# Kernel optimization log

Measured on AMD Instinct MI355X. Metric: run time of the kernel, lower is better.

Reference implementation:

```python
import jax, jax.numpy as jnp
import numpy as np

N_ATOMS = 100_000
N_EDGES = 200_000
N_LG = 400_000
N_GRAPHS = 1024
ATOM_FDIM = 39
BOND_FDIM = 11
HIDDEN = 300
DEPTH = 6


def setup_inputs() -> dict:
    key = jax.random.key(0)
    ks = jax.random.split(key, 10)
    atom_features = jax.random.normal(ks[0], (N_ATOMS, ATOM_FDIM), jnp.float32)
    bond_features = jax.random.normal(ks[1], (N_EDGES, BOND_FDIM), jnp.float32)
    edge_src = jax.random.randint(ks[2], (N_EDGES,), 0, N_ATOMS)
    edge_dst = jax.random.randint(ks[3], (N_EDGES,), 0, N_ATOMS)
    lg_src = jax.random.randint(ks[4], (N_LG,), 0, N_EDGES)
    lg_dst = jax.random.randint(ks[5], (N_LG,), 0, N_EDGES)
    # deterministic balanced assignment of atoms to graphs (every graph non-empty)
    graph_ids = (jnp.arange(N_ATOMS) * N_GRAPHS) // N_ATOMS
    fan_in = ATOM_FDIM + BOND_FDIM
    W_i = jax.random.normal(ks[6], (fan_in, HIDDEN), jnp.float32) * (1.0 / np.sqrt(fan_in))
    W_h = jax.random.normal(ks[7], (HIDDEN, HIDDEN), jnp.float32) * (1.0 / np.sqrt(HIDDEN))
    W_o = jax.random.normal(ks[8], (ATOM_FDIM + HIDDEN, HIDDEN), jnp.float32) * (1.0 / np.sqrt(ATOM_FDIM + HIDDEN))
    b_o = jax.random.normal(ks[9], (HIDDEN,), jnp.float32) * 0.01
    return {
        'atom_features': atom_features, 'bond_features': bond_features,
        'W_i': W_i, 'W_h': W_h, 'W_o': W_o, 'b_o': b_o,
        'edge_src': edge_src, 'edge_dst': edge_dst,
        'lg_src': lg_src, 'lg_dst': lg_dst, 'graph_ids': graph_ids,
    }


def reference(atom_features, bond_features, W_i, W_h, W_o, b_o,
              edge_src, edge_dst, lg_src, lg_dst, graph_ids):
    # line-graph node features: [source atom feats | bond feats] -> W_i
    feats = jnp.concatenate([atom_features[edge_src], bond_features], axis=1)  # [E, 50]
    msg_input = feats @ W_i                                                    # [E, H]
    msg = jax.nn.relu(msg_input)

    # loopy BP: depth-1 iterations of gather-sum over line-graph edges + linear + relu
    def step(msg, _):
        accum = jax.ops.segment_sum(msg[lg_src], lg_dst, num_segments=N_EDGES)  # [E, H]
        return jax.nn.relu(msg_input + accum @ W_h), None
    msg, _ = jax.lax.scan(step, msg, None, length=DEPTH - 1)

    # gather edge messages into destination atoms, then GatherUpdate
    m = jax.ops.segment_sum(msg, edge_dst, num_segments=N_ATOMS)               # [N, H]
    h = jax.nn.relu(jnp.concatenate([atom_features, m], axis=1) @ W_o + b_o)   # [N, H]

    # per-graph mean pooling
    sums = jax.ops.segment_sum(h, graph_ids, num_segments=N_GRAPHS)            # [G, H]
    counts = jax.ops.segment_sum(jnp.ones((N_ATOMS, 1), h.dtype), graph_ids, num_segments=N_GRAPHS)
    return sums / jnp.maximum(counts, 1.0)
```

## Files before the change

### kernel.cpp

```cpp
#include <hip/hip_runtime.h>
#include <stdint.h>

#define NA 100000
#define NE 200000
#define NLG 400000
#define NG 1024
#define AF 39
#define BFD 11
#define HID 300
#define DEPTH 6

#define E_PAD 200064
#define A_PAD 100096
#define EG 12504
#define AGR 6250
#define AG2 6256
#define MS 304
#define NT 20

typedef unsigned short u16;
typedef __attribute__((ext_vector_type(8))) short s8v;
typedef __attribute__((ext_vector_type(8))) unsigned short u16x8;
typedef __attribute__((ext_vector_type(4))) float f4v;

__device__ inline u16 f2bf(float x){
  unsigned u = __float_as_uint(x);
  u += 0x7FFFu + ((u>>16)&1u);
  return (u16)(u>>16);
}
__device__ inline float bf2f(u16 b){ return __uint_as_float(((unsigned)b)<<16); }

#define GLOAD_LDS16(gp, lp) __builtin_amdgcn_global_load_lds( \
    (const __attribute__((address_space(1))) void*)(gp), \
    (__attribute__((address_space(3))) void*)(lp), 16, 0, 0)

__global__ void prep_whi(const float* __restrict__ Wi, const float* __restrict__ Wh,
                         u16* __restrict__ Wf){
  int idx = blockIdx.x*256 + threadIdx.x;
  const int total = 12*NT*512;
  if (idx >= total) return;
  int j    = idx & 7;
  int lane = (idx>>3) & 63;
  int tile = idx >> 9;
  int nt = tile % NT, kt = tile / NT;
  int k = kt*32 + ((lane>>4)<<3) + j;
  int n = nt*16 + (lane&15);
  float v = 0.f;
  if (n < HID){
    if (k < AF+BFD) v = Wi[(size_t)k*HID + n];
    else if (k >= 64 && k < 64+HID) v = Wh[(size_t)(k-64)*HID + n];
  }
  Wf[idx] = f2bf(v);
}

__global__ void prep_wo(const float* __restrict__ W, u16* __restrict__ Wf){
  int idx = blockIdx.x*256 + threadIdx.x;
  const int total = 11*NT*512;
  if (idx >= total) return;
  int j    = idx & 7;
  int lane = (idx>>3) & 63;
  int tile = idx >> 9;
  int nt = tile % NT, kt = tile / NT;
  int k = kt*32 + ((lane>>4)<<3) + j;
  int n = nt*16 + (lane&15);
  int ks = (k < AF) ? k : ((k >= 48 && k < 348) ? (k-9) : -1);
  float v = 0.f;
  if (ks >= 0 && n < HID) v = W[(size_t)ks*HID + n];
  Wf[idx] = f2bf(v);
}

__global__ void hist_k(const int* __restrict__ dst, int* __restrict__ cnt, int n){
  int i = blockIdx.x*256 + threadIdx.x;
  if (i < n) atomicAdd(&cnt[dst[i]], 1);
}
__global__ void scan1(const int* __restrict__ cnt, int* __restrict__ off,
                      int* __restrict__ part, int n){
  __shared__ int s[256];
  const int t = threadIdx.x, b = blockIdx.x;
  const int i0 = b*1024 + t*4;
  int v0 = (i0+0<n)?cnt[i0+0]:0, v1=(i0+1<n)?cnt[i0+1]:0, v2=(i0+2<n)?cnt[i0+2]:0, v3=(i0+3<n)?cnt[i0+3]:0;
  int sum = v0+v1+v2+v3;
  s[t]=sum; __syncthreads();
  for (int o=1;o<256;o<<=1){ int x=(t>=o)?s[t-o]:0; __syncthreads(); s[t]+=x; __syncthreads(); }
  int excl = s[t]-sum;
  if (i0+0<n) off[i0+0]=excl;
  if (i0+1<n) off[i0+1]=excl+v0;
  if (i0+2<n) off[i0+2]=excl+v0+v1;
  if (i0+3<n) off[i0+3]=excl+v0+v1+v2;
  if (t==255) part[b]=s[255];
}
__global__ void scan2(const int* __restrict__ part, int* __restrict__ pref, int nblk){
  __shared__ int s[256];
  const int t = threadIdx.x;
  int v = (t<nblk)?part[t]:0;
  s[t]=v; __syncthreads();
  for (int o=1;o<256;o<<=1){ int x=(t>=o)?s[t-o]:0; __syncthreads(); s[t]+=x; __syncthreads(); }
  pref[t] = s[t]-v;
}
__global__ void scan3(int* __restrict__ off, const int* __restrict__ pref,
                      const int* __restrict__ part, int n, int nblk){
  const int t = threadIdx.x, b = blockIdx.x;
  const int i0 = b*1024 + t*4;
  const int p = pref[b];
  #pragma unroll
  for (int k=0;k<4;++k) if (i0+k<n) off[i0+k]+=p;
  if (b==0 && t==0) off[n] = pref[nblk-1] + part[nblk-1];
}
__global__ void scatter_val(const int* __restrict__ dst, const int* __restrict__ src,
                            const int* __restrict__ off, int* __restrict__ cur,
                            int* __restrict__ csr, int n){
  int i = blockIdx.x*256 + threadIdx.x; if (i>=n) return;
  int d = dst[i];
  int p = off[d] + atomicAdd(&cur[d],1);
  csr[p] = src[i];
}
__global__ void scatter_idx(const int* __restrict__ dst, const int* __restrict__ off,
                            int* __restrict__ cur, int* __restrict__ csr, int n){
  int i = blockIdx.x*256 + threadIdx.x; if (i>=n) return;
  int d = dst[i];
  int p = off[d] + atomicAdd(&cur[d],1);
  csr[p] = i;
}

__launch_bounds__(256,3)
__global__ void gather_lg_k(const u16* __restrict__ msg, u16* __restrict__ accf,
                            const int* __restrict__ off, const int* __restrict__ csr){
  const int w = threadIdx.x>>6, lane = threadIdx.x&63;
  const int g16 = blockIdx.x*4 + w;
  if (g16 >= EG) return;
  const int e = g16*16 + (lane&15);
  const int gc = lane>>4;
  int s=0, epos=0;
  if (e < NE){ s = off[e]; epos = off[e+1]; }
  float acc[10][8];
  #pragma unroll
  for (int c=0;c<10;++c)
    #pragma unroll
    for (int j=0;j<8;++j) acc[c][j] = 0.f;
  const bool c9live = (gc < 2);
  for (int it=s; it<epos; ++it){
    const int src = csr[it];
    const u16* base = msg + (size_t)src*MS + gc*8;
    u16x8 v[10];
    #pragma unroll
    for (int c=0;c<9;++c) v[c] = *(const u16x8*)(base + c*32);
    if (c9live) v[9] = *(const u16x8*)(base + 288);
    else { u16x8 z = {0,0,0,0,0,0,0,0}; v[9] = z; }
    #pragma unroll
    for (int c=0;c<10;++c)
      #pragma unroll
      for (int j=0;j<8;++j) acc[c][j] += bf2f(v[c][j]);
  }
  #pragma unroll
  for (int c=0;c<10;++c){
    u16x8 o;
    #pragma unroll
    for (int j=0;j<8;++j) o[j] = f2bf(acc[c][j]);
    *(u16x8*)(accf + ((size_t)g16*10 + c)*512 + lane*8) = o;
  }
}

__launch_bounds__(256,3)
__global__ void gather_at_k(const u16* __restrict__ msg, const float* __restrict__ atomf,
                            u16* __restrict__ atf,
                            const int* __restrict__ off, const int* __restrict__ csr){
  const int w = threadIdx.x>>6, lane = threadIdx.x&63;
  const int g16 = blockIdx.x*4 + w;
  if (g16 >= AGR) return;
  const int a = g16*16 + (lane&15);
  const int gc = lane>>4;
  const int s = off[a], epos = off[a+1];
  float acc[10][8];
  #pragma unroll
  for (int c=0;c<10;++c)
    #pragma unroll
    for (int j=0;j<8;++j) acc[c][j] = 0.f;
  const bool k1live = (gc >= 2);
  for (int it=s; it<epos; ++it){
    const int src = csr[it];
    const u16* base = msg + (size_t)src*MS + gc*8 - 48;
    u16x8 v[10];
    if (k1live) v[0] = *(const u16x8*)(base + 32);
    else { u16x8 z = {0,0,0,0,0,0,0,0}; v[0] = z; }
    #pragma unroll
    for (int kt=2; kt<=10; ++kt) v[kt-1] = *(const u16x8*)(base + kt*32);
    #pragma unroll
    for (int c=0;c<10;++c)
      #pragma unroll
      for (int j=0;j<8;++j) acc[c][j] += bf2f(v[c][j]);
  }
  #pragma unroll
  for (int kt=1; kt<=10; ++kt){
    u16x8 o;
    if (kt==1 && !k1live){
      #pragma unroll
      for (int j=0;j<8;++j){
        const int k = 32 + gc*8 + j;
        o[j] = f2bf((k < AF) ? atomf[(size_t)a*AF + k] : 0.f);
      }
    } else {
      #pragma unroll
      for (int j=0;j<8;++j) o[j] = f2bf(acc[kt-1][j]);
    }
    *(u16x8*)(atf + ((size_t)g16*11 + kt)*512 + lane*8) = o;
  }
}

__global__ void prep_atom(const float* __restrict__ atomf, u16* __restrict__ atf){
  const int w = threadIdx.x>>6, lane = threadIdx.x&63;
  const int g16 = blockIdx.x*4 + w;
  if (g16 >= AGR) return;
  const int a = g16*16 + (lane&15);
  const int gc = lane>>4;
  u16x8 o;
  #pragma unroll
  for (int j=0;j<8;++j) o[j] = f2bf(atomf[(size_t)a*AF + gc*8 + j]);
  *(u16x8*)(atf + ((size_t)g16*11 + 0)*512 + lane*8) = o;
}

template<int MODE>
__launch_bounds__(256,2)
__global__ void gemm_fused(const float* __restrict__ atomf,
                           const float* __restrict__ bondf,
                           const int*   __restrict__ esrc,
                           const u16*   __restrict__ Afrag,
                           const u16*   __restrict__ Bfrag,
                           u16*         __restrict__ msgout,
                           const float* __restrict__ bo,
                           const int*   __restrict__ gids,
                           float*       __restrict__ gout)
{
  constexpr int KT = (MODE==0) ? 2 : (MODE==1 ? 12 : 11);
  __shared__ u16 lds[2][28*512];
  const int t = threadIdx.x, w = t>>6, lane = t&63;
  const int wr = w>>1, wc = w&1;
  const int m0g = blockIdx.x*8;
  const int r16 = lane&15, gc = lane>>4;

  int rowv[2], srcv[2];
  #pragma unroll
  for (int i=0;i<2;++i){
    const int row = (m0g + w*2 + i)*16 + r16;
    rowv[i] = row;
    if constexpr (MODE<=1) srcv[i] = (row < NE) ? esrc[row] : 0;
    else                   srcv[i] = 0;
  }

  f4v acc[4][10];
  const f4v fz = {0.f,0.f,0.f,0.f};
  #pragma unroll
  for (int i=0;i<4;++i)
    #pragma unroll
    for (int n=0;n<10;++n) acc[i][n] = fz;

  auto stageA = [&](int buf, int kt){
    if constexpr (MODE==2){
      #pragma unroll
      for (int i=0;i<2;++i){
        const int rg = m0g + w*2 + i;
        GLOAD_LDS16(Afrag + ((size_t)rg*11 + kt)*512 + lane*8, &lds[buf][(w*2+i)*512]);
      }
    } else {
      if (MODE==1 && kt >= 2){
        #pragma unroll
        for (int i=0;i<2;++i){
          const int rg = m0g + w*2 + i;
          GLOAD_LDS16(Afrag + ((size_t)rg*10 + (kt-2))*512 + lane*8, &lds[buf][(w*2+i)*512]);
        }
      } else {
        #pragma unroll
        for (int i=0;i<2;++i){
          const int row = rowv[i];
          const int src = srcv[i];
          const bool ok = row < NE;
          const int k0  = kt*32 + gc*8;
          u16x8 o;
          #pragma unroll
          for (int j=0;j<8;++j){
            const int k = k0+j;
            float x = 0.f;
            if (ok){
              if (k < AF) x = atomf[(size_t)src*AF + k];
              else if (k < AF+BFD) x = bondf[(size_t)row*BFD + (k-AF)];
            }
            o[j] = f2bf(x);
          }
          *(u16x8*)(&lds[buf][(w*2+i)*512 + lane*8]) = o;
        }
      }
    }
    #pragma unroll
    for (int i=0;i<5;++i){
      const int nt = w*5+i;
      GLOAD_LDS16(Bfrag + ((size_t)kt*NT + nt)*512 + lane*8, &lds[buf][(8+nt)*512]);
    }
  };

  int buf = 0;
  stageA(0, 0);
  __syncthreads();
  for (int kt=0; kt<KT; ++kt){
    if (kt+1 < KT) stageA(buf^1, kt+1);
    s8v a[4];
    #pragma unroll
    for (int i=0;i<4;++i) a[i] = *(const s8v*)&lds[buf][(wr*4+i)*512 + lane*8];
    #pragma unroll
    for (int h2=0; h2<2; ++h2){
      s8v b[5];
      #pragma unroll
      for (int n=0;n<5;++n) b[n] = *(const s8v*)&lds[buf][(8 + wc*10 + h2*5 + n)*512 + lane*8];
      #pragma unroll
      for (int n=0;n<5;++n)
        #pragma unroll
        for (int i=0;i<4;++i)
          acc[i][h2*5+n] = __builtin_amdgcn_mfma_f32_16x16x32_bf16(a[i], b[n], acc[i][h2*5+n], 0,0,0);
    }
    __syncthreads();
    buf ^= 1;
  }

  const int colL = r16;
  const int row0 = m0g*16 + wr*64 + (gc<<2);
  if constexpr (MODE<=1){
    #pragma unroll
    for (int n=0;n<10;++n){
      const int col = wc*160 + n*16 + colL;
      if (col >= MS) continue;
      #pragma unroll
      for (int i=0;i<4;++i)
        #pragma unroll
        for (int r=0;r<4;++r){
          const int row = row0 + i*16 + r;
          const float v = (col < HID) ? fmaxf(acc[i][n][r], 0.f) : 0.f;
          msgout[(size_t)row*MS + col] = f2bf(v);
        }
    }
  } else {
    float* pl = (float*)&lds[0][0];
    for (int idx=t; idx<960; idx+=256) pl[idx] = 0.f;
    __syncthreads();
    const int gb = gids[m0g*16 < NA ? m0g*16 : (NA-1)];
    #pragma unroll
    for (int n=0;n<10;++n){
      const int col = wc*160 + n*16 + colL;
      if (col >= HID) continue;
      const float bv = bo[col];
      #pragma unroll
      for (int i=0;i<4;++i)
        #pragma unroll
        for (int r=0;r<4;++r){
          const int row = row0 + i*16 + r;
          if (row >= NA) continue;
          const float h = fmaxf(acc[i][n][r] + bv, 0.f);
          const int gl = gids[row] - gb;
          atomicAdd(&pl[gl*320 + col], h);
        }
    }
    __syncthreads();
    for (int idx=t; idx<960; idx+=256){
      const int g = idx/320, c = idx - g*320;
      if (c < HID){
        const int gg = gb + g;
        if (gg < NG){
          const float vv = pl[idx];
          if (vv != 0.f) atomicAdd(&gout[(size_t)gg*HID + c], vv);
        }
      }
    }
  }
}

__device__ inline int lbound(const int* a, int n, int v){
  int lo=0, hi=n;
  while (lo<hi){ int m=(lo+hi)>>1; if (a[m]<v) lo=m+1; else hi=m; }
  return lo;
}
__global__ void scale_k(float* __restrict__ out, const int* __restrict__ gids){
  const int g = blockIdx.x, t = threadIdx.x;
  __shared__ int se[2];
  if (t < 2) se[t] = lbound(gids, NA, g+t);
  __syncthreads();
  const float inv = 1.0f / (float)((se[1]-se[0]) > 1 ? (se[1]-se[0]) : 1);
  for (int c=t; c<HID; c+=256)
    out[(size_t)g*HID + c] *= inv;
}

extern "C" void kernel_launch(void* const* d_in, const int* in_sizes, int n_in,
                              void* d_out, int out_size, void* d_ws, size_t ws_size,
                              hipStream_t stream)
{
  const float* atomf = (const float*)d_in[0];
  const float* bondf = (const float*)d_in[1];
  const float* W_i   = (const float*)d_in[2];
  const float* W_h   = (const float*)d_in[3];
  const float* W_o   = (const float*)d_in[4];
  const float* b_o   = (const float*)d_in[5];
  const int*   esrc  = (const int*)d_in[6];
  const int*   edst  = (const int*)d_in[7];
  const int*   lsrc  = (const int*)d_in[8];
  const int*   ldst  = (const int*)d_in[9];
  const int*   gids  = (const int*)d_in[10];

  char* ws = (char*)d_ws;
  size_t wsoff = 0;
  auto walloc = [&](size_t bytes)->void*{
    void* p = ws + wsoff;
    wsoff += (bytes + 1023) & ~(size_t)1023;
    return p;
  };
  u16*  m0    = (u16*) walloc((size_t)E_PAD*MS*2);
  u16*  m1    = (u16*) walloc((size_t)EG*10*1024);
  u16*  atf   = m1;
  u16*  whif  = (u16*) walloc((size_t)12*NT*512*2);
  u16*  wof   = (u16*) walloc((size_t)11*NT*512*2);
  int* off_lg = (int*) walloc((size_t)(NE+1)*4);
  int* csr_lg = (int*) walloc((size_t)NLG*4);
  int* buf_lg = (int*) walloc((size_t)NE*4);
  int* off_at = (int*) walloc((size_t)(NA+1)*4);
  int* csr_at = (int*) walloc((size_t)NE*4);
  int* buf_at = (int*) walloc((size_t)NA*4);
  int* part1  = (int*) walloc(256*4);
  int* pref1  = (int*) walloc(256*4);
  int* part2  = (int*) walloc(256*4);
  int* pref2  = (int*) walloc(256*4);

  if (wsoff > ws_size) return;

  float* gout = (float*)d_out;
  hipMemsetAsync(gout,   0, (size_t)out_size*4, stream);
  hipMemsetAsync(buf_lg, 0, (size_t)NE*4, stream);
  hipMemsetAsync(buf_at, 0, (size_t)NA*4, stream);

  prep_whi<<<480,256,0,stream>>>(W_i, W_h, whif);
  prep_wo <<<440,256,0,stream>>>(W_o, wof);

  hist_k<<<(NLG+255)/256,256,0,stream>>>(ldst, buf_lg, NLG);
  hist_k<<<(NE+255)/256,256,0,stream>>>(edst, buf_at, NE);
  scan1<<<196,256,0,stream>>>(buf_lg, off_lg, part1, NE);
  scan2<<<1,256,0,stream>>>(part1, pref1, 196);
  scan3<<<196,256,0,stream>>>(off_lg, pref1, part1, NE, 196);
  scan1<<<98,256,0,stream>>>(buf_at, off_at, part2, NA);
  scan2<<<1,256,0,stream>>>(part2, pref2, 98);
  scan3<<<98,256,0,stream>>>(off_at, pref2, part2, NA, 98);
  hipMemsetAsync(buf_lg, 0, (size_t)NE*4, stream);
  hipMemsetAsync(buf_at, 0, (size_t)NA*4, stream);
  scatter_val<<<(NLG+255)/256,256,0,stream>>>(ldst, lsrc, off_lg, buf_lg, csr_lg, NLG);
  scatter_idx<<<(NE+255)/256,256,0,stream>>>(edst, off_at, buf_at, csr_at, NE);

  gemm_fused<0><<<E_PAD/128,256,0,stream>>>(atomf, bondf, esrc, nullptr, whif, m0,
                                            nullptr, nullptr, nullptr);

  for (int d=0; d<DEPTH-1; ++d){
    gather_lg_k<<<EG/4,256,0,stream>>>(m0, m1, off_lg, csr_lg);
    gemm_fused<1><<<E_PAD/128,256,0,stream>>>(atomf, bondf, esrc, m1, whif, m0,
                                              nullptr, nullptr, nullptr);
  }

  prep_atom  <<<(AGR+3)/4,256,0,stream>>>(atomf, atf);
  gather_at_k<<<(AGR+3)/4,256,0,stream>>>(m0, atomf, atf, off_at, csr_at);
  gemm_fused<2><<<A_PAD/128,256,0,stream>>>(atomf, bondf, nullptr, atf, wof, nullptr,
                                            b_o, gids, gout);

  scale_k<<<NG,256,0,stream>>>(gout, gids);
}
```

Before: 1.295 ms.

## Load MFMA fragments directly from global into registers and stage output through LDS

Replaces the LDS double-buffered GEMM with one that loads pre-swizzled A and B fragments straight from global memory into registers, fully unrolls the K loop, and prefetches the first two edge-feature K tiles into registers up front. The message-output epilogue now transposes through per-wave LDS so each lane writes contiguous 16-byte row chunks instead of scattered 2-byte stores. Launch bounds drop to one block per SM, allowing more registers. The aim is to remove block-wide barriers and LDS traffic and to coalesce the output writes, at the cost of redundant B-fragment global/L2 reads across waves and possibly lower occupancy.

New measurement: 1.781 ms. +37.6%, slower.

```diff
diff --git a/kernel.cpp b/kernel.cpp
--- a/kernel.cpp
+++ b/kernel.cpp
@@ -14,7 +14,6 @@
 #define A_PAD 100096
 #define EG 12504
 #define AGR 6250
-#define AG2 6256
 #define MS 304
 #define NT 20
 
@@ -29,10 +28,6 @@
   return (u16)(u>>16);
 }
 __device__ inline float bf2f(u16 b){ return __uint_as_float(((unsigned)b)<<16); }
-
-#define GLOAD_LDS16(gp, lp) __builtin_amdgcn_global_load_lds( \
-    (const __attribute__((address_space(1))) void*)(gp), \
-    (__attribute__((address_space(3))) void*)(lp), 16, 0, 0)
 
 __global__ void prep_whi(const float* __restrict__ Wi, const float* __restrict__ Wh,
                          u16* __restrict__ Wf){
@@ -219,33 +214,24 @@
 }
 
 template<int MODE>
-__launch_bounds__(256,2)
-__global__ void gemm_fused(const float* __restrict__ atomf,
-                           const float* __restrict__ bondf,
-                           const int*   __restrict__ esrc,
-                           const u16*   __restrict__ Afrag,
-                           const u16*   __restrict__ Bfrag,
-                           u16*         __restrict__ msgout,
-                           const float* __restrict__ bo,
-                           const int*   __restrict__ gids,
-                           float*       __restrict__ gout)
+__launch_bounds__(256,1)
+__global__ void gemm_reg(const float* __restrict__ atomf,
+                         const float* __restrict__ bondf,
+                         const int*   __restrict__ esrc,
+                         const u16*   __restrict__ Afrag,
+                         const u16*   __restrict__ Bfrag,
+                         u16*         __restrict__ msgout,
+                         const float* __restrict__ bo,
+                         const int*   __restrict__ gids,
+                         float*       __restrict__ gout)
 {
   constexpr int KT = (MODE==0) ? 2 : (MODE==1 ? 12 : 11);
-  __shared__ u16 lds[2][28*512];
+  __shared__ u16 smem[4*64*88];
   const int t = threadIdx.x, w = t>>6, lane = t&63;
   const int wr = w>>1, wc = w&1;
   const int m0g = blockIdx.x*8;
   const int r16 = lane&15, gc = lane>>4;
 
-  int rowv[2], srcv[2];
-  #pragma unroll
-  for (int i=0;i<2;++i){
-    const int row = (m0g + w*2 + i)*16 + r16;
-    rowv[i] = row;
-    if constexpr (MODE<=1) srcv[i] = (row < NE) ? esrc[row] : 0;
-    else                   srcv[i] = 0;
-  }
-
   f4v acc[4][10];
   const f4v fz = {0.f,0.f,0.f,0.f};
   #pragma unroll
@@ -253,93 +239,103 @@
     #pragma unroll
     for (int n=0;n<10;++n) acc[i][n] = fz;
 
-  auto stageA = [&](int buf, int kt){
-    if constexpr (MODE==2){
-      #pragma unroll
-      for (int i=0;i<2;++i){
-        const int rg = m0g + w*2 + i;
-        GLOAD_LDS16(Afrag + ((size_t)rg*11 + kt)*512 + lane*8, &lds[buf][(w*2+i)*512]);
-      }
-    } else {
-      if (MODE==1 && kt >= 2){
+  s8v fa[2][4];
+  if constexpr (MODE<=1){
+    #pragma unroll
+    for (int i=0;i<4;++i){
+      const int rg  = m0g + wr*4 + i;
+      const int row = rg*16 + r16;
+      const bool ok = row < NE;
+      const int src = ok ? esrc[row] : 0;
+      #pragma unroll
+      for (int kt=0; kt<2; ++kt){
+        u16x8 o;
         #pragma unroll
-        for (int i=0;i<2;++i){
-          const int rg = m0g + w*2 + i;
-          GLOAD_LDS16(Afrag + ((size_t)rg*10 + (kt-2))*512 + lane*8, &lds[buf][(w*2+i)*512]);
+        for (int j=0;j<8;++j){
+          const int k = kt*32 + gc*8 + j;
+          float x = 0.f;
+          if (ok){
+            if (k < AF) x = atomf[(size_t)src*AF + k];
+            else if (k < AF+BFD) x = bondf[(size_t)row*BFD + (k-AF)];
+          }
+          o[j] = f2bf(x);
         }
+        fa[kt][i] = (s8v)o;
+      }
+    }
+  }
+
+  #pragma unroll
+  for (int kt=0; kt<KT; ++kt){
+    s8v a[4];
+    #pragma unroll
+    for (int i=0;i<4;++i){
+      const int rg = m0g + wr*4 + i;
+      if constexpr (MODE==2){
+        a[i] = *(const s8v*)(Afrag + ((size_t)rg*11 + kt)*512 + lane*8);
+      } else if constexpr (MODE==1){
+        if (kt < 2) a[i] = fa[kt][i];
+        else        a[i] = *(const s8v*)(Afrag + ((size_t)rg*10 + (kt-2))*512 + lane*8);
       } else {
-        #pragma unroll
-        for (int i=0;i<2;++i){
-          const int row = rowv[i];
-          const int src = srcv[i];
-          const bool ok = row < NE;
-          const int k0  = kt*32 + gc*8;
-          u16x8 o;
-          #pragma unroll
-          for (int j=0;j<8;++j){
-            const int k = k0+j;
-            float x = 0.f;
-            if (ok){
-              if (k < AF) x = atomf[(size_t)src*AF + k];
-              else if (k < AF+BFD) x = bondf[(size_t)row*BFD + (k-AF)];
-            }
-            o[j] = f2bf(x);
-          }
-          *(u16x8*)(&lds[buf][(w*2+i)*512 + lane*8]) = o;
-        }
-      }
-    }
-    #pragma unroll
-    for (int i=0;i<5;++i){
-      const int nt = w*5+i;
-      GLOAD_LDS16(Bfrag + ((size_t)kt*NT + nt)*512 + lane*8, &lds[buf][(8+nt)*512]);
-    }
-  };
-
-  int buf = 0;
-  stageA(0, 0);
-  __syncthreads();
-  for (int kt=0; kt<KT; ++kt){
-    if (kt+1 < KT) stageA(buf^1, kt+1);
-    s8v a[4];
-    #pragma unroll
-    for (int i=0;i<4;++i) a[i] = *(const s8v*)&lds[buf][(wr*4+i)*512 + lane*8];
+        a[i] = fa[kt][i];
+      }
+    }
     #pragma unroll
     for (int h2=0; h2<2; ++h2){
       s8v b[5];
       #pragma unroll
-      for (int n=0;n<5;++n) b[n] = *(const s8v*)&lds[buf][(8 + wc*10 + h2*5 + n)*512 + lane*8];
+      for (int n=0;n<5;++n){
+        const int nt = wc*10 + h2*5 + n;
+        b[n] = *(const s8v*)(Bfrag + ((size_t)kt*NT + nt)*512 + lane*8);
+      }
       #pragma unroll
       for (int n=0;n<5;++n)
         #pragma unroll
         for (int i=0;i<4;++i)
           acc[i][h2*5+n] = __builtin_amdgcn_mfma_f32_16x16x32_bf16(a[i], b[n], acc[i][h2*5+n], 0,0,0);
     }
+  }
+
+  if constexpr (MODE<=1){
+    u16* sm = smem + w*64*88;
+    const int grow0 = m0g*16 + wr*64;
+    #pragma unroll
+    for (int h=0; h<2; ++h){
+      #pragma unroll
+      for (int n5=0; n5<5; ++n5){
+        const int n    = h*5 + n5;
+        const int colg = wc*160 + n*16 + r16;
+        #pragma unroll
+        for (int i=0;i<4;++i)
+          #pragma unroll
+          for (int r=0;r<4;++r){
+            const int row_l = (gc<<2) + i*16 + r;
+            const float v = (colg < HID) ? fmaxf(acc[i][n][r], 0.f) : 0.f;
+            sm[row_l*88 + n5*16 + r16] = f2bf(v);
+          }
+      }
+      asm volatile("s_waitcnt lgkmcnt(0)" ::: "memory");
+      __builtin_amdgcn_sched_barrier(0);
+      const int cbase = wc*160 + h*80;
+      #pragma unroll
+      for (int q=0;q<10;++q){
+        const int c0 = cbase + q*8;
+        if (c0 < MS){
+          u16x8 v = *(u16x8*)&sm[lane*88 + q*8];
+          *(u16x8*)(msgout + (size_t)(grow0 + lane)*MS + c0) = v;
+        }
+      }
+      asm volatile("s_waitcnt lgkmcnt(0)" ::: "memory");
+      __builtin_amdgcn_sched_barrier(0);
+    }
+  } else {
+    float* pl = (float*)smem;
     __syncthreads();
-    buf ^= 1;
-  }
-
-  const int colL = r16;
-  const int row0 = m0g*16 + wr*64 + (gc<<2);
-  if constexpr (MODE<=1){
-    #pragma unroll
-    for (int n=0;n<10;++n){
-      const int col = wc*160 + n*16 + colL;
-      if (col >= MS) continue;
-      #pragma unroll
-      for (int i=0;i<4;++i)
-        #pragma unroll
-        for (int r=0;r<4;++r){
-          const int row = row0 + i*16 + r;
-          const float v = (col < HID) ? fmaxf(acc[i][n][r], 0.f) : 0.f;
-          msgout[(size_t)row*MS + col] = f2bf(v);
-        }
-    }
-  } else {
-    float* pl = (float*)&lds[0][0];
     for (int idx=t; idx<960; idx+=256) pl[idx] = 0.f;
     __syncthreads();
     const int gb = gids[m0g*16 < NA ? m0g*16 : (NA-1)];
+    const int colL = r16;
+    const int row0 = m0g*16 + wr*64 + (gc<<2);
     #pragma unroll
     for (int n=0;n<10;++n){
       const int col = wc*160 + n*16 + colL;
@@ -447,19 +443,19 @@
   scatter_val<<<(NLG+255)/256,256,0,stream>>>(ldst, lsrc, off_lg, buf_lg, csr_lg, NLG);
   scatter_idx<<<(NE+255)/256,256,0,stream>>>(edst, off_at, buf_at, csr_at, NE);
 
-  gemm_fused<0><<<E_PAD/128,256,0,stream>>>(atomf, bondf, esrc, nullptr, whif, m0,
-                                            nullptr, nullptr, nullptr);
+  gemm_reg<0><<<E_PAD/128,256,0,stream>>>(atomf, bondf, esrc, nullptr, whif, m0,
+                                          nullptr, nullptr, nullptr);
 
   for (int d=0; d<DEPTH-1; ++d){
     gather_lg_k<<<EG/4,256,0,stream>>>(m0, m1, off_lg, csr_lg);
-    gemm_fused<1><<<E_PAD/128,256,0,stream>>>(atomf, bondf, esrc, m1, whif, m0,
-                                              nullptr, nullptr, nullptr);
+    gemm_reg<1><<<E_PAD/128,256,0,stream>>>(atomf, bondf, esrc, m1, whif, m0,
+                                            nullptr, nullptr, nullptr);
   }
 
   prep_atom  <<<(AGR+3)/4,256,0,stream>>>(atomf, atf);
   gather_at_k<<<(AGR+3)/4,256,0,stream>>>(m0, atomf, atf, off_at, csr_at);
-  gemm_fused<2><<<A_PAD/128,256,0,stream>>>(atomf, bondf, nullptr, atf, wof, nullptr,
-                                            b_o, gids, gout);
+  gemm_reg<2><<<A_PAD/128,256,0,stream>>>(atomf, bondf, nullptr, atf, wof, nullptr,
+                                          b_o, gids, gout);
 
   scale_k<<<NG,256,0,stream>>>(gout, gids);
 }
```
